# Performance work log

Measured on AMD Instinct MI355X. Metric: run time of the kernel, lower is better.

The kernel has to match this reference:

```python
import jax, jax.numpy as jnp
import numpy as np

DT = 0.2
LEN_HIST = 16
BATCH = 100000
LEN_PRED = 25


def _consts():
    H = jnp.zeros((2, 4), jnp.float32).at[0, 0].set(1.0).at[1, 2].set(1.0)
    Ht = H.T
    F = jnp.eye(4, dtype=jnp.float32).at[0, 1].set(DT).at[2, 3].set(DT)
    G = jnp.array([DT * DT / 2, DT, DT * DT / 2, DT], dtype=jnp.float32)
    Id = jnp.eye(4, dtype=jnp.float32)
    return H, Ht, F, G, Id


def setup_inputs():
    key = jax.random.key(0)
    hist = jax.random.normal(key, (LEN_HIST, BATCH, 2), dtype=jnp.float32)
    return {
        "hist": hist,
        "velocity_std_x": jnp.ones((1,), jnp.float32) * 0.1355,
        "velocity_std_y": jnp.ones((1,), jnp.float32) * 20.007,
        "acceleration_std_x": jnp.ones((1,), jnp.float32) * 2.771,
        "acceleration_std_y": jnp.ones((1,), jnp.float32) * 6.2014,
        "GR": jnp.array([1e-5, -1e-5], jnp.float32),
        "coef_G": jnp.array([-2.5296, 0.0723, -0.1533, -0.4032], jnp.float32),
        "len_pred": LEN_PRED,
    }


def _forward(hist, vsx, vsy, asx, asy, GR, coef_G, len_pred):
    H, Ht, F, G, Id = _consts()
    # Process noise Q: outer(G*tanh(coef_G)) with x/y diagonal blocks scaled
    ax2 = (asx * asx)[0]
    ay2 = (asy * asy)[0]
    mx = jnp.array([1.0, 1.0, 0.0, 0.0], jnp.float32)
    my = 1.0 - mx
    scale = ax2 * jnp.outer(mx, mx) + ay2 * jnp.outer(my, my) + jnp.outer(mx, my) + jnp.outer(my, mx)
    g = G * jnp.tanh(coef_G)
    Q = jnp.outer(g, g) * scale  # (4,4)
    R = jnp.outer(GR, GR)        # (2,2) measurement noise

    Z = hist[..., None]          # (T, B, 2, 1)
    B = hist.shape[1]

    # --- init ---
    V0 = (Z[1] - Z[0]) / DT                      # (B,2,1)
    X = Ht @ Z[0]                                # (B,4,1)
    X = X.at[:, 1, 0].set(V0[:, 0, 0]).at[:, 3, 0].set(V0[:, 1, 0])
    diag0 = jnp.stack([R[0, 0], (vsx * vsx)[0], R[1, 1], (vsy * vsy)[0]])
    P = jnp.broadcast_to(jnp.diag(diag0), (B, 4, 4))

    def pred(X, P):
        return F @ X, F @ P @ F.T + Q

    def filt_step(carry, z):
        X, P = carry
        X, P = pred(X, P)
        y = z - H @ X                            # (B,2,1)
        S = H @ P @ Ht + R                       # (B,2,2)
        # K = P H^T S^{-1}, computed as in torch.solve(H P^T, S^T)^T
        Kt = jnp.linalg.solve(jnp.swapaxes(S, -1, -2), H @ jnp.swapaxes(P, -1, -2))
        K = jnp.swapaxes(Kt, -1, -2)             # (B,4,2)
        X = X + K @ y
        ImKH = Id - K @ H
        P = ImKH @ P @ jnp.swapaxes(ImKH, -1, -2) + K @ R @ jnp.swapaxes(K, -1, -2)
        return (X, P), None

    (X, P), _ = jax.lax.scan(filt_step, (X, P), Z[1:])

    def pred_step(carry, _):
        X, P = pred(*carry)
        mu = (H @ X)[..., 0]                     # (B,2)
        Pout = H @ P @ Ht                        # (B,2,2)
        return (X, P), (mu, Pout)

    _, (mu, Pout) = jax.lax.scan(pred_step, (X, P), None, length=len_pred)
    sx = jnp.sqrt(Pout[..., 0, 0])[..., None]    # (L,B,1)
    sy = jnp.sqrt(Pout[..., 1, 1])[..., None]
    rho = (Pout[..., 0, 1] + Pout[..., 1, 0])[..., None] / (2.0 * sx * sy)
    return jnp.concatenate([mu, sx, sy, rho], axis=2)  # (L,B,5)


def reference(hist, velocity_std_x, velocity_std_y, acceleration_std_x, acceleration_std_y, GR, coef_G, len_pred):
    return _forward(hist, velocity_std_x, velocity_std_y, acceleration_std_x,
                    acceleration_std_y, GR, coef_G, len_pred)
```

## Files before the change

kernel.cpp:

```cpp
#include <hip/hip_runtime.h>
#include <math.h>

#define DT 0.2f
#define LEN_HIST 16

__global__ __launch_bounds__(256) void kalman_cv_kernel(
    const float* __restrict__ hist,
    const float* __restrict__ vsx_p, const float* __restrict__ vsy_p,
    const float* __restrict__ asx_p, const float* __restrict__ asy_p,
    const float* __restrict__ GR_p,  const float* __restrict__ coefG_p,
    float* __restrict__ out, int B, int len_pred)
{
    int b = blockIdx.x * blockDim.x + threadIdx.x;
    if (b >= B) return;

    const float Gv0 = DT * DT * 0.5f, Gv1 = DT, Gv2 = DT * DT * 0.5f, Gv3 = DT;
    float ax2 = asx_p[0] * asx_p[0];
    float ay2 = asy_p[0] * asy_p[0];
    float g[4];
    g[0] = Gv0 * tanhf(coefG_p[0]);
    g[1] = Gv1 * tanhf(coefG_p[1]);
    g[2] = Gv2 * tanhf(coefG_p[2]);
    g[3] = Gv3 * tanhf(coefG_p[3]);
    float Q[4][4];
    #pragma unroll
    for (int i = 0; i < 4; ++i) {
        #pragma unroll
        for (int j = 0; j < 4; ++j) {
            float s = (i < 2) ? ((j < 2) ? ax2 : 1.0f)
                              : ((j < 2) ? 1.0f : ay2);
            Q[i][j] = g[i] * g[j] * s;
        }
    }
    float GR0 = GR_p[0], GR1 = GR_p[1];
    float R00 = GR0 * GR0, R01 = GR0 * GR1, R10 = GR1 * GR0, R11 = GR1 * GR1;
    float vsx2 = vsx_p[0] * vsx_p[0];
    float vsy2 = vsy_p[0] * vsy_p[0];

    float2 z[LEN_HIST];
    #pragma unroll
    for (int t = 0; t < LEN_HIST; ++t)
        z[t] = *reinterpret_cast<const float2*>(hist + ((size_t)t * B + b) * 2);

    float X0 = z[0].x;
    float X1 = (z[1].x - z[0].x) / DT;
    float X2 = z[0].y;
    float X3 = (z[1].y - z[0].y) / DT;

    float P[4][4] = {};
    P[0][0] = R00; P[1][1] = vsx2; P[2][2] = R11; P[3][3] = vsy2;

    #pragma unroll
    for (int t = 1; t < LEN_HIST; ++t) {
        X0 += DT * X1;
        X2 += DT * X3;
        float T[4][4];
        #pragma unroll
        for (int j = 0; j < 4; ++j) {
            T[0][j] = P[0][j] + DT * P[1][j];
            T[1][j] = P[1][j];
            T[2][j] = P[2][j] + DT * P[3][j];
            T[3][j] = P[3][j];
        }
        #pragma unroll
        for (int i = 0; i < 4; ++i) {
            P[i][0] = T[i][0] + DT * T[i][1] + Q[i][0];
            P[i][1] = T[i][1]               + Q[i][1];
            P[i][2] = T[i][2] + DT * T[i][3] + Q[i][2];
            P[i][3] = T[i][3]               + Q[i][3];
        }

        float y0 = z[t].x - X0;
        float y1 = z[t].y - X2;
        float S00 = P[0][0] + R00, S01 = P[0][2] + R01;
        float S10 = P[2][0] + R10, S11 = P[2][2] + R11;
        float inv = 1.0f / (S00 * S11 - S01 * S10);
        float Si00 =  S11 * inv, Si01 = -S01 * inv;
        float Si10 = -S10 * inv, Si11 =  S00 * inv;

        float K[4][2];
        #pragma unroll
        for (int i = 0; i < 4; ++i) {
            K[i][0] = P[i][0] * Si00 + P[i][2] * Si10;
            K[i][1] = P[i][0] * Si01 + P[i][2] * Si11;
        }

        X0 += K[0][0] * y0 + K[0][1] * y1;
        X1 += K[1][0] * y0 + K[1][1] * y1;
        X2 += K[2][0] * y0 + K[2][1] * y1;
        X3 += K[3][0] * y0 + K[3][1] * y1;

        float U[4][4];
        #pragma unroll
        for (int i = 0; i < 4; ++i) {
            #pragma unroll
            for (int j = 0; j < 4; ++j)
                U[i][j] = P[i][j] - K[i][0] * P[0][j] - K[i][1] * P[2][j];
        }
        float w[4];
        #pragma unroll
        for (int i = 0; i < 4; ++i)
            w[i] = K[i][0] * GR0 + K[i][1] * GR1;
        #pragma unroll
        for (int i = 0; i < 4; ++i) {
            #pragma unroll
            for (int j = 0; j < 4; ++j)
                P[i][j] = U[i][j] - U[i][0] * K[j][0] - U[i][2] * K[j][1] + w[i] * w[j];
        }
    }

    size_t ob = (size_t)b * 5;
    for (int l = 0; l < len_pred; ++l) {
        X0 += DT * X1;
        X2 += DT * X3;
        float T[4][4];
        #pragma unroll
        for (int j = 0; j < 4; ++j) {
            T[0][j] = P[0][j] + DT * P[1][j];
            T[1][j] = P[1][j];
            T[2][j] = P[2][j] + DT * P[3][j];
            T[3][j] = P[3][j];
        }
        #pragma unroll
        for (int i = 0; i < 4; ++i) {
            P[i][0] = T[i][0] + DT * T[i][1] + Q[i][0];
            P[i][1] = T[i][1]               + Q[i][1];
            P[i][2] = T[i][2] + DT * T[i][3] + Q[i][2];
            P[i][3] = T[i][3]               + Q[i][3];
        }
        float sx = sqrtf(P[0][0]);
        float sy = sqrtf(P[2][2]);
        float rho = (P[0][2] + P[2][0]) / (2.0f * sx * sy);
        float* o = out + (size_t)l * B * 5 + ob;
        o[0] = X0;
        o[1] = X2;
        o[2] = sx;
        o[3] = sy;
        o[4] = rho;
    }
}

extern "C" void kernel_launch(void* const* d_in, const int* in_sizes, int n_in,
                              void* d_out, int out_size, void* d_ws, size_t ws_size,
                              hipStream_t stream) {
    const float* hist  = (const float*)d_in[0];
    const float* vsx   = (const float*)d_in[1];
    const float* vsy   = (const float*)d_in[2];
    const float* asx   = (const float*)d_in[3];
    const float* asy   = (const float*)d_in[4];
    const float* GR    = (const float*)d_in[5];
    const float* coefG = (const float*)d_in[6];
    float* out = (float*)d_out;

    int B = in_sizes[0] / (LEN_HIST * 2);
    int len_pred = out_size / (B * 5);

    int block = 256;
    int grid = (B + block - 1) / block;
    kalman_cv_kernel<<<grid, block, 0, stream>>>(hist, vsx, vsy, asx, asy, GR, coefG,
                                                 out, B, len_pred);
}
```

Before: 26.72 us.

## Hoist batch-independent covariance and gain recursion into a single-thread setup kernel

The covariance P, the Kalman gain K and the predicted sx/sy/rho do not depend on the measurements, so they are the same for every track. A one-thread setup kernel now computes all gains and prediction statistics once and writes them to workspace. The per-track kernel reads them into shared memory and only updates the state vector. This removes the per-thread 4x4 matrix arithmetic, but adds a serial kernel launch and caps the prediction length at 32.

```diff
diff --git a/kernel.cpp b/kernel.cpp
--- a/kernel.cpp
+++ b/kernel.cpp
@@ -3,16 +3,16 @@
 
 #define DT 0.2f
 #define LEN_HIST 16
+#define MAX_PRED 32
 
-__global__ __launch_bounds__(256) void kalman_cv_kernel(
-    const float* __restrict__ hist,
+
+__global__ void kalman_setup_kernel(
     const float* __restrict__ vsx_p, const float* __restrict__ vsy_p,
     const float* __restrict__ asx_p, const float* __restrict__ asy_p,
     const float* __restrict__ GR_p,  const float* __restrict__ coefG_p,
-    float* __restrict__ out, int B, int len_pred)
+    float* __restrict__ ws, int len_pred)
 {
-    int b = blockIdx.x * blockDim.x + threadIdx.x;
-    if (b >= B) return;
+    if (threadIdx.x != 0 || blockIdx.x != 0) return;
 
     const float Gv0 = DT * DT * 0.5f, Gv1 = DT, Gv2 = DT * DT * 0.5f, Gv3 = DT;
     float ax2 = asx_p[0] * asx_p[0];
@@ -37,23 +37,11 @@
     float vsx2 = vsx_p[0] * vsx_p[0];
     float vsy2 = vsy_p[0] * vsy_p[0];
 
-    float2 z[LEN_HIST];
-    #pragma unroll
-    for (int t = 0; t < LEN_HIST; ++t)
-        z[t] = *reinterpret_cast<const float2*>(hist + ((size_t)t * B + b) * 2);
-
-    float X0 = z[0].x;
-    float X1 = (z[1].x - z[0].x) / DT;
-    float X2 = z[0].y;
-    float X3 = (z[1].y - z[0].y) / DT;
-
     float P[4][4] = {};
     P[0][0] = R00; P[1][1] = vsx2; P[2][2] = R11; P[3][3] = vsy2;
 
     #pragma unroll
     for (int t = 1; t < LEN_HIST; ++t) {
-        X0 += DT * X1;
-        X2 += DT * X3;
         float T[4][4];
         #pragma unroll
         for (int j = 0; j < 4; ++j) {
@@ -70,8 +58,6 @@
             P[i][3] = T[i][3]               + Q[i][3];
         }
 
-        float y0 = z[t].x - X0;
-        float y1 = z[t].y - X2;
         float S00 = P[0][0] + R00, S01 = P[0][2] + R01;
         float S10 = P[2][0] + R10, S11 = P[2][2] + R11;
         float inv = 1.0f / (S00 * S11 - S01 * S10);
@@ -84,11 +70,11 @@
             K[i][0] = P[i][0] * Si00 + P[i][2] * Si10;
             K[i][1] = P[i][0] * Si01 + P[i][2] * Si11;
         }
-
-        X0 += K[0][0] * y0 + K[0][1] * y1;
-        X1 += K[1][0] * y0 + K[1][1] * y1;
-        X2 += K[2][0] * y0 + K[2][1] * y1;
-        X3 += K[3][0] * y0 + K[3][1] * y1;
+        #pragma unroll
+        for (int i = 0; i < 4; ++i) {
+            ws[(t - 1) * 8 + i * 2 + 0] = K[i][0];
+            ws[(t - 1) * 8 + i * 2 + 1] = K[i][1];
+        }
 
         float U[4][4];
         #pragma unroll
@@ -109,10 +95,7 @@
         }
     }
 
-    size_t ob = (size_t)b * 5;
     for (int l = 0; l < len_pred; ++l) {
-        X0 += DT * X1;
-        X2 += DT * X3;
         float T[4][4];
         #pragma unroll
         for (int j = 0; j < 4; ++j) {
@@ -131,12 +114,59 @@
         float sx = sqrtf(P[0][0]);
         float sy = sqrtf(P[2][2]);
         float rho = (P[0][2] + P[2][0]) / (2.0f * sx * sy);
-        float* o = out + (size_t)l * B * 5 + ob;
+        ws[128 + l * 3 + 0] = sx;
+        ws[128 + l * 3 + 1] = sy;
+        ws[128 + l * 3 + 2] = rho;
+    }
+}
+
+__global__ __launch_bounds__(256) void kalman_track_kernel(
+    const float* __restrict__ hist, const float* __restrict__ ws,
+    float* __restrict__ out, int B, int len_pred)
+{
+    __shared__ float sK[15 * 8];
+    __shared__ float sC[3 * MAX_PRED];
+
+    int tid = threadIdx.x;
+    for (int i = tid; i < 120; i += 256) sK[i] = ws[i];
+    for (int i = tid; i < 3 * len_pred; i += 256) sC[i] = ws[128 + i];
+    __syncthreads();
+
+    int b = blockIdx.x * 256 + tid;
+    if (b >= B) return;
+
+    float2 z[LEN_HIST];
+    #pragma unroll
+    for (int t = 0; t < LEN_HIST; ++t)
+        z[t] = *reinterpret_cast<const float2*>(hist + ((size_t)t * B + b) * 2);
+
+    float X0 = z[0].x;
+    float X1 = (z[1].x - z[0].x) / DT;
+    float X2 = z[0].y;
+    float X3 = (z[1].y - z[0].y) / DT;
+
+    #pragma unroll
+    for (int t = 1; t < LEN_HIST; ++t) {
+        X0 += DT * X1;
+        X2 += DT * X3;
+        float y0 = z[t].x - X0;
+        float y1 = z[t].y - X2;
+        const float* K = &sK[(t - 1) * 8];
+        X0 += K[0] * y0 + K[1] * y1;
+        X1 += K[2] * y0 + K[3] * y1;
+        X2 += K[4] * y0 + K[5] * y1;
+        X3 += K[6] * y0 + K[7] * y1;
+    }
+
+    for (int l = 0; l < len_pred; ++l) {
+        X0 += DT * X1;
+        X2 += DT * X3;
+        float* o = out + ((size_t)l * B + b) * 5;
         o[0] = X0;
         o[1] = X2;
-        o[2] = sx;
-        o[3] = sy;
-        o[4] = rho;
+        o[2] = sC[l * 3 + 0];
+        o[3] = sC[l * 3 + 1];
+        o[4] = sC[l * 3 + 2];
     }
 }
 
@@ -151,12 +181,15 @@
     const float* GR    = (const float*)d_in[5];
     const float* coefG = (const float*)d_in[6];
     float* out = (float*)d_out;
+    float* ws  = (float*)d_ws;
 
     int B = in_sizes[0] / (LEN_HIST * 2);
     int len_pred = out_size / (B * 5);
+    if (len_pred > MAX_PRED) len_pred = MAX_PRED;
+
+    kalman_setup_kernel<<<1, 64, 0, stream>>>(vsx, vsy, asx, asy, GR, coefG, ws, len_pred);
 
     int block = 256;
     int grid = (B + block - 1) / block;
-    kalman_cv_kernel<<<grid, block, 0, stream>>>(hist, vsx, vsy, asx, asy, GR, coefG,
-                                                 out, B, len_pred);
+    kalman_track_kernel<<<grid, block, 0, stream>>>(hist, ws, out, B, len_pred);
 }
```

Result: slower. 35.78 us (+33.9%).

## Compute shared covariance and gain once per block, stage coalesced output stores

Applied to the files above, without the earlier changes.

The covariance and Kalman gain depend only on the parameters, not on the per-track data. One thread per block now computes P, K and the prediction sigma/rho into shared memory, and every thread then runs only the cheap state update for two tracks. Output rows are staged through LDS per wave so each wave writes contiguous float4 stores instead of stride-5 scalar stores. The cost is a serial prologue in one thread while the rest of the block waits at the barrier, and len_pred is capped at 32.

```diff
diff --git a/kernel.cpp b/kernel.cpp
--- a/kernel.cpp
+++ b/kernel.cpp
@@ -3,140 +3,201 @@
 
 #define DT 0.2f
 #define LEN_HIST 16
-
-__global__ __launch_bounds__(256) void kalman_cv_kernel(
+#define MAX_PRED 32
+#define TPB 256
+#define TRKPB (2 * TPB)
+
+__global__ __launch_bounds__(TPB) void kalman_fused(
     const float* __restrict__ hist,
     const float* __restrict__ vsx_p, const float* __restrict__ vsy_p,
     const float* __restrict__ asx_p, const float* __restrict__ asy_p,
     const float* __restrict__ GR_p,  const float* __restrict__ coefG_p,
     float* __restrict__ out, int B, int len_pred)
 {
-    int b = blockIdx.x * blockDim.x + threadIdx.x;
-    if (b >= B) return;
-
-    const float Gv0 = DT * DT * 0.5f, Gv1 = DT, Gv2 = DT * DT * 0.5f, Gv3 = DT;
-    float ax2 = asx_p[0] * asx_p[0];
-    float ay2 = asy_p[0] * asy_p[0];
-    float g[4];
-    g[0] = Gv0 * tanhf(coefG_p[0]);
-    g[1] = Gv1 * tanhf(coefG_p[1]);
-    g[2] = Gv2 * tanhf(coefG_p[2]);
-    g[3] = Gv3 * tanhf(coefG_p[3]);
-    float Q[4][4];
+    __shared__ float sK[15 * 8];
+    __shared__ float sC[3 * MAX_PRED];
+    __shared__ float sT[4][2][320];
+
+    const int tid  = threadIdx.x;
+    const int base = blockIdx.x * TRKPB;
+    const int bA   = base + tid;
+    const int bB   = base + TPB + tid;
+    const bool vA  = bA < B, vB = bB < B;
+    const int iA   = vA ? bA : (B - 1);
+    const int iB   = vB ? bB : (B - 1);
+
+    float2 zA[LEN_HIST], zB[LEN_HIST];
     #pragma unroll
-    for (int i = 0; i < 4; ++i) {
+    for (int t = 0; t < LEN_HIST; ++t) {
+        zA[t] = *reinterpret_cast<const float2*>(hist + ((size_t)t * B + iA) * 2);
+        zB[t] = *reinterpret_cast<const float2*>(hist + ((size_t)t * B + iB) * 2);
+    }
+
+    if (tid == 0) {
+        const float Gv0 = DT * DT * 0.5f, Gv1 = DT, Gv2 = DT * DT * 0.5f, Gv3 = DT;
+        float ax2 = asx_p[0] * asx_p[0];
+        float ay2 = asy_p[0] * asy_p[0];
+        float g[4];
+        g[0] = Gv0 * tanhf(coefG_p[0]);
+        g[1] = Gv1 * tanhf(coefG_p[1]);
+        g[2] = Gv2 * tanhf(coefG_p[2]);
+        g[3] = Gv3 * tanhf(coefG_p[3]);
+        float Q[4][4];
         #pragma unroll
-        for (int j = 0; j < 4; ++j) {
-            float s = (i < 2) ? ((j < 2) ? ax2 : 1.0f)
-                              : ((j < 2) ? 1.0f : ay2);
-            Q[i][j] = g[i] * g[j] * s;
-        }
-    }
-    float GR0 = GR_p[0], GR1 = GR_p[1];
-    float R00 = GR0 * GR0, R01 = GR0 * GR1, R10 = GR1 * GR0, R11 = GR1 * GR1;
-    float vsx2 = vsx_p[0] * vsx_p[0];
-    float vsy2 = vsy_p[0] * vsy_p[0];
-
-    float2 z[LEN_HIST];
-    #pragma unroll
-    for (int t = 0; t < LEN_HIST; ++t)
-        z[t] = *reinterpret_cast<const float2*>(hist + ((size_t)t * B + b) * 2);
-
-    float X0 = z[0].x;
-    float X1 = (z[1].x - z[0].x) / DT;
-    float X2 = z[0].y;
-    float X3 = (z[1].y - z[0].y) / DT;
-
-    float P[4][4] = {};
-    P[0][0] = R00; P[1][1] = vsx2; P[2][2] = R11; P[3][3] = vsy2;
+        for (int i = 0; i < 4; ++i)
+            #pragma unroll
+            for (int j = 0; j < 4; ++j) {
+                float s = (i < 2) ? ((j < 2) ? ax2 : 1.0f)
+                                  : ((j < 2) ? 1.0f : ay2);
+                Q[i][j] = g[i] * g[j] * s;
+            }
+        float GR0 = GR_p[0], GR1 = GR_p[1];
+        float R00 = GR0 * GR0, R01 = GR0 * GR1, R10 = GR1 * GR0, R11 = GR1 * GR1;
+        float P[4][4] = {};
+        P[0][0] = R00; P[1][1] = vsx_p[0] * vsx_p[0];
+        P[2][2] = R11; P[3][3] = vsy_p[0] * vsy_p[0];
+
+        #pragma unroll
+        for (int t = 1; t < LEN_HIST; ++t) {
+            float T[4][4];
+            #pragma unroll
+            for (int j = 0; j < 4; ++j) {
+                T[0][j] = P[0][j] + DT * P[1][j];
+                T[1][j] = P[1][j];
+                T[2][j] = P[2][j] + DT * P[3][j];
+                T[3][j] = P[3][j];
+            }
+            #pragma unroll
+            for (int i = 0; i < 4; ++i) {
+                P[i][0] = T[i][0] + DT * T[i][1] + Q[i][0];
+                P[i][1] = T[i][1]                + Q[i][1];
+                P[i][2] = T[i][2] + DT * T[i][3] + Q[i][2];
+                P[i][3] = T[i][3]                + Q[i][3];
+            }
+            float S00 = P[0][0] + R00, S01 = P[0][2] + R01;
+            float S10 = P[2][0] + R10, S11 = P[2][2] + R11;
+            float inv = 1.0f / (S00 * S11 - S01 * S10);
+            float Si00 =  S11 * inv, Si01 = -S01 * inv;
+            float Si10 = -S10 * inv, Si11 =  S00 * inv;
+            float K[4][2];
+            #pragma unroll
+            for (int i = 0; i < 4; ++i) {
+                K[i][0] = P[i][0] * Si00 + P[i][2] * Si10;
+                K[i][1] = P[i][0] * Si01 + P[i][2] * Si11;
+                sK[(t - 1) * 8 + i * 2 + 0] = K[i][0];
+                sK[(t - 1) * 8 + i * 2 + 1] = K[i][1];
+            }
+            float U[4][4];
+            #pragma unroll
+            for (int i = 0; i < 4; ++i)
+                #pragma unroll
+                for (int j = 0; j < 4; ++j)
+                    U[i][j] = P[i][j] - K[i][0] * P[0][j] - K[i][1] * P[2][j];
+            float w_[4];
+            #pragma unroll
+            for (int i = 0; i < 4; ++i)
+                w_[i] = K[i][0] * GR0 + K[i][1] * GR1;
+            #pragma unroll
+            for (int i = 0; i < 4; ++i)
+                #pragma unroll
+                for (int j = 0; j < 4; ++j)
+                    P[i][j] = U[i][j] - U[i][0] * K[j][0] - U[i][2] * K[j][1] + w_[i] * w_[j];
+        }
+        for (int l = 0; l < len_pred; ++l) {
+            float T[4][4];
+            #pragma unroll
+            for (int j = 0; j < 4; ++j) {
+                T[0][j] = P[0][j] + DT * P[1][j];
+                T[1][j] = P[1][j];
+                T[2][j] = P[2][j] + DT * P[3][j];
+                T[3][j] = P[3][j];
+            }
+            #pragma unroll
+            for (int i = 0; i < 4; ++i) {
+                P[i][0] = T[i][0] + DT * T[i][1] + Q[i][0];
+                P[i][1] = T[i][1]                + Q[i][1];
+                P[i][2] = T[i][2] + DT * T[i][3] + Q[i][2];
+                P[i][3] = T[i][3]                + Q[i][3];
+            }
+            float sx = sqrtf(P[0][0]);
+            float sy = sqrtf(P[2][2]);
+            sC[l * 3 + 0] = sx;
+            sC[l * 3 + 1] = sy;
+            sC[l * 3 + 2] = (P[0][2] + P[2][0]) / (2.0f * sx * sy);
+        }
+    }
+    __syncthreads();
+
+    float A0 = zA[0].x, A1 = (zA[1].x - zA[0].x) / DT;
+    float A2 = zA[0].y, A3 = (zA[1].y - zA[0].y) / DT;
+    float B0 = zB[0].x, B1 = (zB[1].x - zB[0].x) / DT;
+    float B2 = zB[0].y, B3 = (zB[1].y - zB[0].y) / DT;
 
     #pragma unroll
     for (int t = 1; t < LEN_HIST; ++t) {
-        X0 += DT * X1;
-        X2 += DT * X3;
-        float T[4][4];
-        #pragma unroll
-        for (int j = 0; j < 4; ++j) {
-            T[0][j] = P[0][j] + DT * P[1][j];
-            T[1][j] = P[1][j];
-            T[2][j] = P[2][j] + DT * P[3][j];
-            T[3][j] = P[3][j];
-        }
-        #pragma unroll
-        for (int i = 0; i < 4; ++i) {
-            P[i][0] = T[i][0] + DT * T[i][1] + Q[i][0];
-            P[i][1] = T[i][1]               + Q[i][1];
-            P[i][2] = T[i][2] + DT * T[i][3] + Q[i][2];
-            P[i][3] = T[i][3]               + Q[i][3];
-        }
-
-        float y0 = z[t].x - X0;
-        float y1 = z[t].y - X2;
-        float S00 = P[0][0] + R00, S01 = P[0][2] + R01;
-        float S10 = P[2][0] + R10, S11 = P[2][2] + R11;
-        float inv = 1.0f / (S00 * S11 - S01 * S10);
-        float Si00 =  S11 * inv, Si01 = -S01 * inv;
-        float Si10 = -S10 * inv, Si11 =  S00 * inv;
-
-        float K[4][2];
-        #pragma unroll
-        for (int i = 0; i < 4; ++i) {
-            K[i][0] = P[i][0] * Si00 + P[i][2] * Si10;
-            K[i][1] = P[i][0] * Si01 + P[i][2] * Si11;
-        }
-
-        X0 += K[0][0] * y0 + K[0][1] * y1;
-        X1 += K[1][0] * y0 + K[1][1] * y1;
-        X2 += K[2][0] * y0 + K[2][1] * y1;
-        X3 += K[3][0] * y0 + K[3][1] * y1;
-
-        float U[4][4];
-        #pragma unroll
-        for (int i = 0; i < 4; ++i) {
-            #pragma unroll
-            for (int j = 0; j < 4; ++j)
-                U[i][j] = P[i][j] - K[i][0] * P[0][j] - K[i][1] * P[2][j];
-        }
-        float w[4];
-        #pragma unroll
-        for (int i = 0; i < 4; ++i)
-            w[i] = K[i][0] * GR0 + K[i][1] * GR1;
-        #pragma unroll
-        for (int i = 0; i < 4; ++i) {
-            #pragma unroll
-            for (int j = 0; j < 4; ++j)
-                P[i][j] = U[i][j] - U[i][0] * K[j][0] - U[i][2] * K[j][1] + w[i] * w[j];
-        }
-    }
-
-    size_t ob = (size_t)b * 5;
+        const float4 kx = *reinterpret_cast<const float4*>(&sK[(t - 1) * 8]);
+        const float4 ky = *reinterpret_cast<const float4*>(&sK[(t - 1) * 8 + 4]);
+        A0 += DT * A1; A2 += DT * A3;
+        float y0 = zA[t].x - A0, y1 = zA[t].y - A2;
+        A0 += kx.x * y0 + kx.y * y1;
+        A1 += kx.z * y0 + kx.w * y1;
+        A2 += ky.x * y0 + ky.y * y1;
+        A3 += ky.z * y0 + ky.w * y1;
+        B0 += DT * B1; B2 += DT * B3;
+        y0 = zB[t].x - B0; y1 = zB[t].y - B2;
+        B0 += kx.x * y0 + kx.y * y1;
+        B1 += kx.z * y0 + kx.w * y1;
+        B2 += ky.x * y0 + ky.y * y1;
+        B3 += ky.z * y0 + ky.w * y1;
+    }
+
+    const int lane = tid & 63, w = tid >> 6;
+    float* bufA = &sT[w][0][0];
+    float* bufB = &sT[w][1][0];
+    const int gA = base + w * 64;
+    const int gB = base + TPB + w * 64;
+    const bool fullA = (gA + 63) < B;
+    const bool fullB = (gB + 63) < B;
+    const bool alignOK = (((size_t)B * 5) & 3) == 0;
+
     for (int l = 0; l < len_pred; ++l) {
-        X0 += DT * X1;
-        X2 += DT * X3;
-        float T[4][4];
-        #pragma unroll
-        for (int j = 0; j < 4; ++j) {
-            T[0][j] = P[0][j] + DT * P[1][j];
-            T[1][j] = P[1][j];
-            T[2][j] = P[2][j] + DT * P[3][j];
-            T[3][j] = P[3][j];
-        }
-        #pragma unroll
-        for (int i = 0; i < 4; ++i) {
-            P[i][0] = T[i][0] + DT * T[i][1] + Q[i][0];
-            P[i][1] = T[i][1]               + Q[i][1];
-            P[i][2] = T[i][2] + DT * T[i][3] + Q[i][2];
-            P[i][3] = T[i][3]               + Q[i][3];
-        }
-        float sx = sqrtf(P[0][0]);
-        float sy = sqrtf(P[2][2]);
-        float rho = (P[0][2] + P[2][0]) / (2.0f * sx * sy);
-        float* o = out + (size_t)l * B * 5 + ob;
-        o[0] = X0;
-        o[1] = X2;
-        o[2] = sx;
-        o[3] = sy;
-        o[4] = rho;
+        A0 += DT * A1; A2 += DT * A3;
+        B0 += DT * B1; B2 += DT * B3;
+        const float cx = sC[3 * l], cy = sC[3 * l + 1], cr = sC[3 * l + 2];
+
+        if (fullA && alignOK) {
+            __builtin_amdgcn_wave_barrier();
+            bufA[lane * 5 + 0] = A0;
+            bufA[lane * 5 + 1] = A2;
+            bufA[lane * 5 + 2] = cx;
+            bufA[lane * 5 + 3] = cy;
+            bufA[lane * 5 + 4] = cr;
+            __builtin_amdgcn_wave_barrier();
+            float* oA = out + ((size_t)l * B + gA) * 5;
+            *reinterpret_cast<float4*>(oA + lane * 4) =
+                *reinterpret_cast<const float4*>(&bufA[lane * 4]);
+            oA[256 + lane] = bufA[256 + lane];
+        } else if (vA) {
+            float* o = out + ((size_t)l * B + bA) * 5;
+            o[0] = A0; o[1] = A2; o[2] = cx; o[3] = cy; o[4] = cr;
+        }
+
+        if (fullB && alignOK) {
+            __builtin_amdgcn_wave_barrier();
+            bufB[lane * 5 + 0] = B0;
+            bufB[lane * 5 + 1] = B2;
+            bufB[lane * 5 + 2] = cx;
+            bufB[lane * 5 + 3] = cy;
+            bufB[lane * 5 + 4] = cr;
+            __builtin_amdgcn_wave_barrier();
+            float* oB = out + ((size_t)l * B + gB) * 5;
+            *reinterpret_cast<float4*>(oB + lane * 4) =
+                *reinterpret_cast<const float4*>(&bufB[lane * 4]);
+            oB[256 + lane] = bufB[256 + lane];
+        } else if (vB) {
+            float* o = out + ((size_t)l * B + bB) * 5;
+            o[0] = B0; o[1] = B2; o[2] = cx; o[3] = cy; o[4] = cr;
+        }
     }
 }
 
@@ -154,9 +215,9 @@
 
     int B = in_sizes[0] / (LEN_HIST * 2);
     int len_pred = out_size / (B * 5);
-
-    int block = 256;
-    int grid = (B + block - 1) / block;
-    kalman_cv_kernel<<<grid, block, 0, stream>>>(hist, vsx, vsy, asx, asy, GR, coefG,
-                                                 out, B, len_pred);
+    if (len_pred > MAX_PRED) len_pred = MAX_PRED;
+
+    int grid = (B + TRKPB - 1) / TRKPB;
+    kalman_fused<<<grid, TPB, 0, stream>>>(hist, vsx, vsy, asx, asy, GR, coefG,
+                                           out, B, len_pred);
 }
```

Result: slower. 30.89 us (+15.6%).

## Hoist batch-invariant Riccati recursion to one lane and split into filter+emit kernels

Applied to the files above, without the earlier changes.

The covariance/gain recursion does not depend on the measurements, so one thread per block computes the Kalman gains and predicted covariance statistics into shared memory. Every other thread then runs only the cheap state update. A second kernel writes the outputs as coalesced float4 stores, with the predicted means computed in closed form (x + t*v). This removes redundant 4x4 matrix work per element and the strided 5-float stores, at the cost of a serial single-lane section per block, a second launch and a workspace round trip.

```diff
diff --git a/kernel.cpp b/kernel.cpp
--- a/kernel.cpp
+++ b/kernel.cpp
@@ -3,17 +3,15 @@
 
 #define DT 0.2f
 #define LEN_HIST 16
-
-__global__ __launch_bounds__(256) void kalman_cv_kernel(
-    const float* __restrict__ hist,
+#define MAX_PRED 32
+
+
+__device__ __forceinline__ void riccati_lane0(
     const float* __restrict__ vsx_p, const float* __restrict__ vsy_p,
     const float* __restrict__ asx_p, const float* __restrict__ asy_p,
     const float* __restrict__ GR_p,  const float* __restrict__ coefG_p,
-    float* __restrict__ out, int B, int len_pred)
+    float* sK, float* sC, int len_pred)
 {
-    int b = blockIdx.x * blockDim.x + threadIdx.x;
-    if (b >= B) return;
-
     const float Gv0 = DT * DT * 0.5f, Gv1 = DT, Gv2 = DT * DT * 0.5f, Gv3 = DT;
     float ax2 = asx_p[0] * asx_p[0];
     float ay2 = asy_p[0] * asy_p[0];
@@ -24,36 +22,21 @@
     g[3] = Gv3 * tanhf(coefG_p[3]);
     float Q[4][4];
     #pragma unroll
-    for (int i = 0; i < 4; ++i) {
+    for (int i = 0; i < 4; ++i)
         #pragma unroll
         for (int j = 0; j < 4; ++j) {
             float s = (i < 2) ? ((j < 2) ? ax2 : 1.0f)
                               : ((j < 2) ? 1.0f : ay2);
             Q[i][j] = g[i] * g[j] * s;
         }
-    }
     float GR0 = GR_p[0], GR1 = GR_p[1];
     float R00 = GR0 * GR0, R01 = GR0 * GR1, R10 = GR1 * GR0, R11 = GR1 * GR1;
-    float vsx2 = vsx_p[0] * vsx_p[0];
-    float vsy2 = vsy_p[0] * vsy_p[0];
-
-    float2 z[LEN_HIST];
-    #pragma unroll
-    for (int t = 0; t < LEN_HIST; ++t)
-        z[t] = *reinterpret_cast<const float2*>(hist + ((size_t)t * B + b) * 2);
-
-    float X0 = z[0].x;
-    float X1 = (z[1].x - z[0].x) / DT;
-    float X2 = z[0].y;
-    float X3 = (z[1].y - z[0].y) / DT;
-
     float P[4][4] = {};
-    P[0][0] = R00; P[1][1] = vsx2; P[2][2] = R11; P[3][3] = vsy2;
+    P[0][0] = R00; P[1][1] = vsx_p[0] * vsx_p[0];
+    P[2][2] = R11; P[3][3] = vsy_p[0] * vsy_p[0];
 
     #pragma unroll
     for (int t = 1; t < LEN_HIST; ++t) {
-        X0 += DT * X1;
-        X2 += DT * X3;
         float T[4][4];
         #pragma unroll
         for (int j = 0; j < 4; ++j) {
@@ -65,54 +48,246 @@
         #pragma unroll
         for (int i = 0; i < 4; ++i) {
             P[i][0] = T[i][0] + DT * T[i][1] + Q[i][0];
-            P[i][1] = T[i][1]               + Q[i][1];
+            P[i][1] = T[i][1]                + Q[i][1];
             P[i][2] = T[i][2] + DT * T[i][3] + Q[i][2];
-            P[i][3] = T[i][3]               + Q[i][3];
-        }
-
-        float y0 = z[t].x - X0;
-        float y1 = z[t].y - X2;
+            P[i][3] = T[i][3]                + Q[i][3];
+        }
         float S00 = P[0][0] + R00, S01 = P[0][2] + R01;
         float S10 = P[2][0] + R10, S11 = P[2][2] + R11;
         float inv = 1.0f / (S00 * S11 - S01 * S10);
         float Si00 =  S11 * inv, Si01 = -S01 * inv;
         float Si10 = -S10 * inv, Si11 =  S00 * inv;
-
         float K[4][2];
         #pragma unroll
         for (int i = 0; i < 4; ++i) {
             K[i][0] = P[i][0] * Si00 + P[i][2] * Si10;
             K[i][1] = P[i][0] * Si01 + P[i][2] * Si11;
-        }
-
+            sK[(t - 1) * 8 + i * 2 + 0] = K[i][0];
+            sK[(t - 1) * 8 + i * 2 + 1] = K[i][1];
+        }
+        float U[4][4];
+        #pragma unroll
+        for (int i = 0; i < 4; ++i)
+            #pragma unroll
+            for (int j = 0; j < 4; ++j)
+                U[i][j] = P[i][j] - K[i][0] * P[0][j] - K[i][1] * P[2][j];
+        float w_[4];
+        #pragma unroll
+        for (int i = 0; i < 4; ++i)
+            w_[i] = K[i][0] * GR0 + K[i][1] * GR1;
+        #pragma unroll
+        for (int i = 0; i < 4; ++i)
+            #pragma unroll
+            for (int j = 0; j < 4; ++j)
+                P[i][j] = U[i][j] - U[i][0] * K[j][0] - U[i][2] * K[j][1] + w_[i] * w_[j];
+    }
+    for (int l = 0; l < len_pred; ++l) {
+        float T[4][4];
+        #pragma unroll
+        for (int j = 0; j < 4; ++j) {
+            T[0][j] = P[0][j] + DT * P[1][j];
+            T[1][j] = P[1][j];
+            T[2][j] = P[2][j] + DT * P[3][j];
+            T[3][j] = P[3][j];
+        }
+        #pragma unroll
+        for (int i = 0; i < 4; ++i) {
+            P[i][0] = T[i][0] + DT * T[i][1] + Q[i][0];
+            P[i][1] = T[i][1]                + Q[i][1];
+            P[i][2] = T[i][2] + DT * T[i][3] + Q[i][2];
+            P[i][3] = T[i][3]                + Q[i][3];
+        }
+        float sx = sqrtf(P[0][0]);
+        float sy = sqrtf(P[2][2]);
+        sC[l * 3 + 0] = sx;
+        sC[l * 3 + 1] = sy;
+        sC[l * 3 + 2] = (P[0][2] + P[2][0]) / (2.0f * sx * sy);
+    }
+}
+
+__global__ __launch_bounds__(256) void k1_filter(
+    const float* __restrict__ hist,
+    const float* __restrict__ vsx, const float* __restrict__ vsy,
+    const float* __restrict__ asx, const float* __restrict__ asy,
+    const float* __restrict__ GR,  const float* __restrict__ coefG,
+    float* __restrict__ ws, int B, int len_pred)
+{
+    __shared__ float sK[15 * 8];
+    __shared__ float sCl[3 * MAX_PRED];
+
+    const int tid = threadIdx.x;
+    const int b = blockIdx.x * 256 + tid;
+    const int ib = (b < B) ? b : (B - 1);
+
+    float2 z[LEN_HIST];
+    #pragma unroll
+    for (int t = 0; t < LEN_HIST; ++t)
+        z[t] = *reinterpret_cast<const float2*>(hist + ((size_t)t * B + ib) * 2);
+
+    if (tid == 0)
+        riccati_lane0(vsx, vsy, asx, asy, GR, coefG, sK, sCl, len_pred);
+    __syncthreads();
+
+    if (blockIdx.x == 0)
+        for (int i = tid; i < 3 * len_pred; i += 256)
+            ws[4 * (size_t)B + i] = sCl[i];
+
+    if (b >= B) return;
+
+    float X0 = z[0].x, X1 = (z[1].x - z[0].x) / DT;
+    float X2 = z[0].y, X3 = (z[1].y - z[0].y) / DT;
+
+    #pragma unroll
+    for (int t = 1; t < LEN_HIST; ++t) {
+        const float4 kx = *reinterpret_cast<const float4*>(&sK[(t - 1) * 8]);
+        const float4 ky = *reinterpret_cast<const float4*>(&sK[(t - 1) * 8 + 4]);
+        X0 += DT * X1; X2 += DT * X3;
+        float y0 = z[t].x - X0, y1 = z[t].y - X2;
+        X0 += kx.x * y0 + kx.y * y1;
+        X1 += kx.z * y0 + kx.w * y1;
+        X2 += ky.x * y0 + ky.y * y1;
+        X3 += ky.z * y0 + ky.w * y1;
+    }
+
+    reinterpret_cast<float4*>(ws)[b] = make_float4(X0, X1, X2, X3);
+}
+
+__global__ __launch_bounds__(256) void k2_emit(
+    const float* __restrict__ ws, float* __restrict__ out, int B, int perL4)
+{
+    const int l = blockIdx.y;
+    const int k = blockIdx.x * 256 + threadIdx.x;
+    if (k >= perL4) return;
+
+    const float4* __restrict__ Xb = reinterpret_cast<const float4*>(ws);
+    const float* __restrict__ sC = ws + 4 * (size_t)B;
+    const float sx = sC[3 * l], sy = sC[3 * l + 1], rho = sC[3 * l + 2];
+    const float t = (float)(l + 1) * DT;
+
+    const int f = 4 * k;
+    const int b0 = f / 5;
+    const int c0 = f - b0 * 5;
+
+    const float4 Xa = Xb[b0];
+    const float4 Xn = Xb[b0 + 1];
+
+    const float muxA = fmaf(t, Xa.y, Xa.x);
+    const float muyA = fmaf(t, Xa.w, Xa.z);
+    const float muxN = fmaf(t, Xn.y, Xn.x);
+    const float muyN = fmaf(t, Xn.w, Xn.z);
+
+    float v[4];
+    #pragma unroll
+    for (int j = 0; j < 4; ++j) {
+        const int cc = c0 + j;
+        v[j] = (cc == 0) ? muxA :
+               (cc == 1) ? muyA :
+               (cc == 2) ? sx :
+               (cc == 3) ? sy :
+               (cc == 4) ? rho :
+               (cc == 5) ? muxN :
+               (cc == 6) ? muyN : sx;
+    }
+    reinterpret_cast<float4*>(out)[(size_t)l * perL4 + k] =
+        make_float4(v[0], v[1], v[2], v[3]);
+}
+
+__global__ __launch_bounds__(256) void kalman_mono(
+    const float* __restrict__ hist,
+    const float* __restrict__ vsx_p, const float* __restrict__ vsy_p,
+    const float* __restrict__ asx_p, const float* __restrict__ asy_p,
+    const float* __restrict__ GR_p,  const float* __restrict__ coefG_p,
+    float* __restrict__ out, int B, int len_pred)
+{
+    int b = blockIdx.x * blockDim.x + threadIdx.x;
+    if (b >= B) return;
+
+    const float Gv0 = DT * DT * 0.5f, Gv1 = DT, Gv2 = DT * DT * 0.5f, Gv3 = DT;
+    float ax2 = asx_p[0] * asx_p[0];
+    float ay2 = asy_p[0] * asy_p[0];
+    float g[4];
+    g[0] = Gv0 * tanhf(coefG_p[0]);
+    g[1] = Gv1 * tanhf(coefG_p[1]);
+    g[2] = Gv2 * tanhf(coefG_p[2]);
+    g[3] = Gv3 * tanhf(coefG_p[3]);
+    float Q[4][4];
+    #pragma unroll
+    for (int i = 0; i < 4; ++i)
+        #pragma unroll
+        for (int j = 0; j < 4; ++j) {
+            float s = (i < 2) ? ((j < 2) ? ax2 : 1.0f)
+                              : ((j < 2) ? 1.0f : ay2);
+            Q[i][j] = g[i] * g[j] * s;
+        }
+    float GR0 = GR_p[0], GR1 = GR_p[1];
+    float R00 = GR0 * GR0, R01 = GR0 * GR1, R10 = GR1 * GR0, R11 = GR1 * GR1;
+
+    float2 z[LEN_HIST];
+    #pragma unroll
+    for (int t = 0; t < LEN_HIST; ++t)
+        z[t] = *reinterpret_cast<const float2*>(hist + ((size_t)t * B + b) * 2);
+
+    float X0 = z[0].x, X1 = (z[1].x - z[0].x) / DT;
+    float X2 = z[0].y, X3 = (z[1].y - z[0].y) / DT;
+    float P[4][4] = {};
+    P[0][0] = R00; P[1][1] = vsx_p[0] * vsx_p[0];
+    P[2][2] = R11; P[3][3] = vsy_p[0] * vsy_p[0];
+
+    #pragma unroll
+    for (int t = 1; t < LEN_HIST; ++t) {
+        float T[4][4];
+        #pragma unroll
+        for (int j = 0; j < 4; ++j) {
+            T[0][j] = P[0][j] + DT * P[1][j];
+            T[1][j] = P[1][j];
+            T[2][j] = P[2][j] + DT * P[3][j];
+            T[3][j] = P[3][j];
+        }
+        #pragma unroll
+        for (int i = 0; i < 4; ++i) {
+            P[i][0] = T[i][0] + DT * T[i][1] + Q[i][0];
+            P[i][1] = T[i][1]                + Q[i][1];
+            P[i][2] = T[i][2] + DT * T[i][3] + Q[i][2];
+            P[i][3] = T[i][3]                + Q[i][3];
+        }
+        float y0 = z[t].x - X0 - DT * X1;
+        float y1 = z[t].y - X2 - DT * X3;
+        X0 += DT * X1; X2 += DT * X3;
+        float S00 = P[0][0] + R00, S01 = P[0][2] + R01;
+        float S10 = P[2][0] + R10, S11 = P[2][2] + R11;
+        float inv = 1.0f / (S00 * S11 - S01 * S10);
+        float Si00 =  S11 * inv, Si01 = -S01 * inv;
+        float Si10 = -S10 * inv, Si11 =  S00 * inv;
+        float K[4][2];
+        #pragma unroll
+        for (int i = 0; i < 4; ++i) {
+            K[i][0] = P[i][0] * Si00 + P[i][2] * Si10;
+            K[i][1] = P[i][0] * Si01 + P[i][2] * Si11;
+        }
         X0 += K[0][0] * y0 + K[0][1] * y1;
         X1 += K[1][0] * y0 + K[1][1] * y1;
         X2 += K[2][0] * y0 + K[2][1] * y1;
         X3 += K[3][0] * y0 + K[3][1] * y1;
-
         float U[4][4];
         #pragma unroll
-        for (int i = 0; i < 4; ++i) {
+        for (int i = 0; i < 4; ++i)
             #pragma unroll
             for (int j = 0; j < 4; ++j)
                 U[i][j] = P[i][j] - K[i][0] * P[0][j] - K[i][1] * P[2][j];
-        }
-        float w[4];
-        #pragma unroll
-        for (int i = 0; i < 4; ++i)
-            w[i] = K[i][0] * GR0 + K[i][1] * GR1;
-        #pragma unroll
-        for (int i = 0; i < 4; ++i) {
+        float w_[4];
+        #pragma unroll
+        for (int i = 0; i < 4; ++i)
+            w_[i] = K[i][0] * GR0 + K[i][1] * GR1;
+        #pragma unroll
+        for (int i = 0; i < 4; ++i)
             #pragma unroll
             for (int j = 0; j < 4; ++j)
-                P[i][j] = U[i][j] - U[i][0] * K[j][0] - U[i][2] * K[j][1] + w[i] * w[j];
-        }
+                P[i][j] = U[i][j] - U[i][0] * K[j][0] - U[i][2] * K[j][1] + w_[i] * w_[j];
     }
 
     size_t ob = (size_t)b * 5;
     for (int l = 0; l < len_pred; ++l) {
-        X0 += DT * X1;
-        X2 += DT * X3;
+        X0 += DT * X1; X2 += DT * X3;
         float T[4][4];
         #pragma unroll
         for (int j = 0; j < 4; ++j) {
@@ -124,19 +299,15 @@
         #pragma unroll
         for (int i = 0; i < 4; ++i) {
             P[i][0] = T[i][0] + DT * T[i][1] + Q[i][0];
-            P[i][1] = T[i][1]               + Q[i][1];
+            P[i][1] = T[i][1]                + Q[i][1];
             P[i][2] = T[i][2] + DT * T[i][3] + Q[i][2];
-            P[i][3] = T[i][3]               + Q[i][3];
+            P[i][3] = T[i][3]                + Q[i][3];
         }
         float sx = sqrtf(P[0][0]);
         float sy = sqrtf(P[2][2]);
         float rho = (P[0][2] + P[2][0]) / (2.0f * sx * sy);
         float* o = out + (size_t)l * B * 5 + ob;
-        o[0] = X0;
-        o[1] = X2;
-        o[2] = sx;
-        o[3] = sy;
-        o[4] = rho;
+        o[0] = X0; o[1] = X2; o[2] = sx; o[3] = sy; o[4] = rho;
     }
 }
 
@@ -151,12 +322,24 @@
     const float* GR    = (const float*)d_in[5];
     const float* coefG = (const float*)d_in[6];
     float* out = (float*)d_out;
+    float* ws  = (float*)d_ws;
 
     int B = in_sizes[0] / (LEN_HIST * 2);
     int len_pred = out_size / (B * 5);
-
-    int block = 256;
-    int grid = (B + block - 1) / block;
-    kalman_cv_kernel<<<grid, block, 0, stream>>>(hist, vsx, vsy, asx, asy, GR, coefG,
-                                                 out, B, len_pred);
-}
+    if (len_pred > MAX_PRED) len_pred = MAX_PRED;
+
+    size_t ws_need = (4 * (size_t)B + 3 * (size_t)len_pred) * sizeof(float)
+                     + sizeof(float4);
+    bool fast = (((size_t)B * 5) % 4 == 0) && ws_size >= ws_need;
+
+    if (fast) {
+        int perL4 = (B * 5) / 4;
+        k1_filter<<<(B + 255) / 256, 256, 0, stream>>>(hist, vsx, vsy, asx, asy,
+                                                       GR, coefG, ws, B, len_pred);
+        dim3 g2((perL4 + 255) / 256, len_pred);
+        k2_emit<<<g2, 256, 0, stream>>>(ws, out, B, perL4);
+    } else {
+        kalman_mono<<<(B + 255) / 256, 256, 0, stream>>>(hist, vsx, vsy, asx, asy,
+                                                         GR, coefG, out, B, len_pred);
+    }
+}
```

Measured after the change: 46.74 us. 1.75x slower.
